# Kernel optimization log

Measured on AMD Instinct MI355X. Metric: run time of the kernel, lower is better.

Reference implementation:

```python
import jax, jax.numpy as jnp
import numpy as np

N, D = 16384, 256

def setup_inputs() -> dict:
    key = jax.random.key(0)
    k1, k2 = jax.random.split(key)
    image_emb = jax.random.normal(k1, (N, D), dtype=jnp.float32)
    text_emb = jax.random.normal(k2, (N, D), dtype=jnp.float32)
    return {"image_emb": image_emb, "text_emb": text_emb}

def reference(image_emb, text_emb):
    n = image_emb.shape[0]
    # [n, n] similarity logits
    logits = image_emb @ text_emb.T
    labels = jnp.arange(n)
    # cross-entropy with diagonal labels: -log_softmax(logits)[i, i]
    logp_t = jax.nn.log_softmax(logits, axis=-1)        # image -> text (rows)
    logp_i = jax.nn.log_softmax(logits.T, axis=-1)      # text -> image (cols)
    loss_t = -logp_t[labels, labels]
    loss_i = -logp_i[labels, labels]
    loss = ((loss_i + loss_t) * 0.5).mean()
    return loss
```

## Files before the change

kernel.cpp:

```cpp
#include <hip/hip_runtime.h>
#include <hip/hip_bf16.h>

#define NN 16384
#define DD 256

typedef unsigned short u16;
typedef unsigned int u32;
typedef unsigned char u8;
typedef long i64;
typedef __attribute__((ext_vector_type(4))) float f32x4;
typedef __attribute__((ext_vector_type(8))) int i32x8;

static __device__ __forceinline__ void gload16(const u8* g, u8* l) {
    __builtin_amdgcn_global_load_lds(
        (const __attribute__((address_space(1))) void*)g,
        (__attribute__((address_space(3))) void*)l,
        16, 0, 0);
}

__global__ void prep_kernel(const float* __restrict__ img, const float* __restrict__ txt,
                            u8* __restrict__ A8, u8* __restrict__ B8,
                            float* __restrict__ zbuf ,
                            float* __restrict__ out) {
    int gid = blockIdx.x * 256 + threadIdx.x;
    float4 va = ((const float4*)img)[gid];
    float4 vb = ((const float4*)txt)[gid];
    const float S = 1.44269504088896f;
    int pa = __builtin_amdgcn_cvt_pk_fp8_f32(va.x * S, va.y * S, 0, false);
    pa     = __builtin_amdgcn_cvt_pk_fp8_f32(va.z * S, va.w * S, pa, true);
    int pb = __builtin_amdgcn_cvt_pk_fp8_f32(vb.x, vb.y, 0, false);
    pb     = __builtin_amdgcn_cvt_pk_fp8_f32(vb.z, vb.w, pb, true);

    const int r  = gid >> 6;
    const int rl = r & 127;
    const int pn = r >> 7;
    const int ko = (gid & 63) << 2;
    const int kb = ko ^ ((rl & 15) << 3);
    *(u32*)(A8 + ((size_t)pn << 15) + (rl << 8) + kb) = (u32)pa;
    *(u32*)(B8 + ((size_t)pn << 15) + (rl << 8) + kb) = (u32)pb;
    if (gid < 32768) zbuf[gid] = 0.0f;
    if (gid == 0) out[0] = 0.0f;
}

__global__ __launch_bounds__(256, 2) void gemm_lse_kernel(
        const u8* __restrict__ A8, const u8* __restrict__ B8,
        float* __restrict__ s_row, float* __restrict__ s_col,
        float* __restrict__ diag) {
    __shared__ u8 sA[32768];
    __shared__ u8 sB[32768];

    const int t = threadIdx.x;
    const int lane = t & 63;
    const int w = t >> 6;
    const int wr = w >> 1, wc = w & 1;
    const int q = lane >> 4, m = lane & 15;
    const int bi = blockIdx.x & 127;
    const int jg = blockIdx.x >> 7;
    const int row0 = bi << 7;

    #pragma unroll
    for (int R = 0; R < 8; ++R)
        gload16(A8 + ((size_t)bi << 15) + (R << 12) + (w << 10) + ((size_t)lane << 4),
                &sA[(R << 12) + (w << 10)]);
    __syncthreads();

    i32x8 areg[2][4];
    #pragma unroll
    for (int k2 = 0; k2 < 2; ++k2)
        #pragma unroll
        for (int rb = 0; rb < 4; ++rb) {
            const int rr = (wr << 6) + (rb << 4) + m;
            union { i32x8 v; i64 d[4]; } ua;
            #pragma unroll
            for (int j = 0; j < 4; ++j)
                ua.d[j] = *(const i64*)(&sA[(rr << 8) + (k2 << 7)
                           + (((q << 5) | (j << 3)) ^ (m << 3))]);
            areg[k2][rb] = ua.v;
        }

    const f32x4 fzero = {0.f, 0.f, 0.f, 0.f};
    const f32x4 cinit = {-144.f, -144.f, -144.f, -144.f};
    f32x4 acc[4][4];
    f32x4 rp[4] = {fzero, fzero, fzero, fzero};

    #pragma unroll 1
    for (int jt = 0; jt < 16; ++jt) {
        const int ct = (jg << 4) | ((jt + bi) & 15);
        const int col0 = ct << 7;
        __syncthreads();
        #pragma unroll
        for (int R = 0; R < 8; ++R)
            gload16(B8 + ((size_t)ct << 15) + (R << 12) + (w << 10) + ((size_t)lane << 4),
                    &sB[(R << 12) + (w << 10)]);
        __syncthreads();

        #pragma unroll
        for (int k2 = 0; k2 < 2; ++k2) {
            i32x8 bf[4];
            #pragma unroll
            for (int cb = 0; cb < 4; ++cb) {
                const int cr = (wc << 6) + (cb << 4) + m;
                union { i32x8 v; i64 d[4]; } ub;
                #pragma unroll
                for (int j = 0; j < 4; ++j)
                    ub.d[j] = *(const i64*)(&sB[(cr << 8) + (k2 << 7)
                               + (((q << 5) | (j << 3)) ^ (m << 3))]);
                bf[cb] = ub.v;
            }
            if (k2 == 0) {
                #pragma unroll
                for (int rb = 0; rb < 4; ++rb)
                    #pragma unroll
                    for (int cb = 0; cb < 4; ++cb)
                        acc[rb][cb] = __builtin_amdgcn_mfma_scale_f32_16x16x128_f8f6f4(
                            areg[0][rb], bf[cb], cinit, 0, 0, 0, 127, 0, 127);
            } else {
                #pragma unroll
                for (int rb = 0; rb < 4; ++rb)
                    #pragma unroll
                    for (int cb = 0; cb < 4; ++cb)
                        acc[rb][cb] = __builtin_amdgcn_mfma_scale_f32_16x16x128_f8f6f4(
                            areg[1][rb], bf[cb], acc[rb][cb], 0, 0, 0, 127, 0, 127);
            }
        }

        if (bi == ct && wr == wc) {
            #pragma unroll
            for (int rb = 0; rb < 4; ++rb)
                #pragma unroll
                for (int r = 0; r < 4; ++r)
                    if (m == ((q << 2) | r))
                        diag[row0 + (wr << 6) + (rb << 4) + m] = acc[rb][rb][r];
        }
        #pragma unroll
        for (int rb = 0; rb < 4; ++rb)
            #pragma unroll
            for (int cb = 0; cb < 4; ++cb)
                #pragma unroll
                for (int r = 0; r < 4; ++r)
                    acc[rb][cb][r] = __builtin_amdgcn_exp2f(acc[rb][cb][r]);

        #pragma unroll
        for (int rb = 0; rb < 4; ++rb)
            rp[rb] += (acc[rb][0] + acc[rb][1]) + (acc[rb][2] + acc[rb][3]);

        float cpart = 0.0f;
        #pragma unroll
        for (int cb = 0; cb < 4; ++cb) {
            float v = 0.0f;
            #pragma unroll
            for (int rb = 0; rb < 4; ++rb)
                v += (acc[rb][cb][0] + acc[rb][cb][1]) + (acc[rb][cb][2] + acc[rb][cb][3]);
            v += __shfl_xor(v, 16, 64);
            v += __shfl_xor(v, 32, 64);
            if (q == cb) cpart = v;
        }
        atomicAdd(&s_col[col0 + (wc << 6) + (q << 4) + m], cpart);
    }

    float rout = 0.0f;
    #pragma unroll
    for (int rb = 0; rb < 4; ++rb)
        #pragma unroll
        for (int r = 0; r < 4; ++r) {
            float v = rp[rb][r];
            v += __shfl_xor(v, 1, 16);
            v += __shfl_xor(v, 2, 16);
            v += __shfl_xor(v, 4, 16);
            v += __shfl_xor(v, 8, 16);
            if (m == ((rb << 2) | r)) rout = v;
        }
    atomicAdd(&s_row[row0 + (wr << 6) + ((m >> 2) << 4) + (q << 2) + (m & 3)], rout);
}

__global__ void final_kernel(const float* __restrict__ s_row, const float* __restrict__ s_col,
                             const float* __restrict__ diag, float* __restrict__ out) {
    __shared__ double red[256];
    int t = threadIdx.x;
    int i = blockIdx.x * 256 + t;
    double p = 0.5 * (double)(log2f(s_row[i]) + log2f(s_col[i])) - (double)diag[i];
    red[t] = p;
    __syncthreads();
    for (int s = 128; s > 0; s >>= 1) {
        if (t < s) red[t] += red[t + s];
        __syncthreads();
    }
    if (t == 0) atomicAdd(out, (float)(red[0] * 0.6931471805599453 / (double)NN));
}

extern "C" void kernel_launch(void* const* d_in, const int* in_sizes, int n_in,
                              void* d_out, int out_size, void* d_ws, size_t ws_size,
                              hipStream_t stream) {
    const float* img = (const float*)d_in[0];
    const float* txt = (const float*)d_in[1];
    char* ws = (char*)d_ws;
    u8*    A8    = (u8*)ws;
    u8*    B8    = (u8*)(ws + 4194304);
    float* s_row = (float*)(ws + 8388608);
    float* s_col = (float*)(ws + 8388608 + 65536);
    float* diag  = (float*)(ws + 8388608 + 131072);
    float* out   = (float*)d_out;

    prep_kernel<<<4096, 256, 0, stream>>>(img, txt, A8, B8, s_row, out);
    gemm_lse_kernel<<<1024, 256, 0, stream>>>(A8, B8, s_row, s_col, diag);
    final_kernel<<<64, 256, 0, stream>>>(s_row, s_col, diag, out);
}
```

Before: 168.9 us.

## Load B fragments directly from global into registers with prefetch, dropping LDS staging

The prep kernel now writes B in a fragment-major layout so each lane can read its MFMA operand with two 16-byte global loads. The GEMM kernel drops the shared B buffer and both per-tile barriers, and instead loads B fragments straight into registers. It prefetches the next tile's first K-half while the current MFMAs run, and raises wave priority around the MFMA blocks. This removes LDS traffic and synchronization, but it raises register pressure and relies on L2 to serve B reuse, since each wave now re-reads B from global memory.

```diff
diff --git a/kernel.cpp b/kernel.cpp
--- a/kernel.cpp
+++ b/kernel.cpp
@@ -9,6 +9,7 @@
 typedef unsigned char u8;
 typedef long i64;
 typedef __attribute__((ext_vector_type(4))) float f32x4;
+typedef __attribute__((ext_vector_type(4))) int i32x4;
 typedef __attribute__((ext_vector_type(8))) int i32x8;
 
 static __device__ __forceinline__ void gload16(const u8* g, u8* l) {
@@ -35,9 +36,13 @@
     const int rl = r & 127;
     const int pn = r >> 7;
     const int ko = (gid & 63) << 2;
-    const int kb = ko ^ ((rl & 15) << 3);
-    *(u32*)(A8 + ((size_t)pn << 15) + (rl << 8) + kb) = (u32)pa;
-    *(u32*)(B8 + ((size_t)pn << 15) + (rl << 8) + kb) = (u32)pb;
+    const int kbA = ko ^ ((rl & 15) << 3);
+    *(u32*)(A8 + ((size_t)pn << 15) + (rl << 8) + kbA) = (u32)pa;
+    const int mm  = rl & 15, cb8 = rl >> 4;
+    const int k2  = ko >> 7, koo = ko & 127;
+    const int qq  = koo >> 5, jj = (koo >> 4) & 1, u = ko & 15;
+    *(u32*)(B8 + ((size_t)pn << 15) + (k2 << 14) + (cb8 << 11) + (jj << 10)
+               + (qq << 8) + (mm << 4) + u) = (u32)pb;
     if (gid < 32768) zbuf[gid] = 0.0f;
     if (gid == 0) out[0] = 0.0f;
 }
@@ -47,7 +52,6 @@
         float* __restrict__ s_row, float* __restrict__ s_col,
         float* __restrict__ diag) {
     __shared__ u8 sA[32768];
-    __shared__ u8 sB[32768];
 
     const int t = threadIdx.x;
     const int lane = t & 63;
@@ -83,46 +87,62 @@
     f32x4 acc[4][4];
     f32x4 rp[4] = {fzero, fzero, fzero, fzero};
 
+    const u8* Bw = B8 + (wc << 13) + ((size_t)lane << 4);
+
+    i32x8 bfA[4], bfB[4];
+
+    {
+        const int ct0 = (jg << 4) | (bi & 15);
+        const u8* p = Bw + ((size_t)ct0 << 15);
+        #pragma unroll
+        for (int cb = 0; cb < 4; ++cb) {
+            i32x4 lo = *(const i32x4*)(p + (cb << 11));
+            i32x4 hi = *(const i32x4*)(p + (cb << 11) + 1024);
+            bfA[cb] = __builtin_shufflevector(lo, hi, 0, 1, 2, 3, 4, 5, 6, 7);
+        }
+    }
+
     #pragma unroll 1
     for (int jt = 0; jt < 16; ++jt) {
         const int ct = (jg << 4) | ((jt + bi) & 15);
         const int col0 = ct << 7;
-        __syncthreads();
-        #pragma unroll
-        for (int R = 0; R < 8; ++R)
-            gload16(B8 + ((size_t)ct << 15) + (R << 12) + (w << 10) + ((size_t)lane << 4),
-                    &sB[(R << 12) + (w << 10)]);
-        __syncthreads();
-
-        #pragma unroll
-        for (int k2 = 0; k2 < 2; ++k2) {
-            i32x8 bf[4];
+        const u8* p = Bw + ((size_t)ct << 15);
+
+        #pragma unroll
+        for (int cb = 0; cb < 4; ++cb) {
+            i32x4 lo = *(const i32x4*)(p + 16384 + (cb << 11));
+            i32x4 hi = *(const i32x4*)(p + 16384 + (cb << 11) + 1024);
+            bfB[cb] = __builtin_shufflevector(lo, hi, 0, 1, 2, 3, 4, 5, 6, 7);
+        }
+
+        __builtin_amdgcn_s_setprio(1);
+        #pragma unroll
+        for (int rb = 0; rb < 4; ++rb)
+            #pragma unroll
+            for (int cb = 0; cb < 4; ++cb)
+                acc[rb][cb] = __builtin_amdgcn_mfma_scale_f32_16x16x128_f8f6f4(
+                    areg[0][rb], bfA[cb], cinit, 0, 0, 0, 127, 0, 127);
+        __builtin_amdgcn_s_setprio(0);
+
+        if (jt < 15) {
+            const int ctn = (jg << 4) | ((jt + 1 + bi) & 15);
+            const u8* pn2 = Bw + ((size_t)ctn << 15);
             #pragma unroll
             for (int cb = 0; cb < 4; ++cb) {
-                const int cr = (wc << 6) + (cb << 4) + m;
-                union { i32x8 v; i64 d[4]; } ub;
-                #pragma unroll
-                for (int j = 0; j < 4; ++j)
-                    ub.d[j] = *(const i64*)(&sB[(cr << 8) + (k2 << 7)
-                               + (((q << 5) | (j << 3)) ^ (m << 3))]);
-                bf[cb] = ub.v;
+                i32x4 lo = *(const i32x4*)(pn2 + (cb << 11));
+                i32x4 hi = *(const i32x4*)(pn2 + (cb << 11) + 1024);
+                bfA[cb] = __builtin_shufflevector(lo, hi, 0, 1, 2, 3, 4, 5, 6, 7);
             }
-            if (k2 == 0) {
-                #pragma unroll
-                for (int rb = 0; rb < 4; ++rb)
-                    #pragma unroll
-                    for (int cb = 0; cb < 4; ++cb)
-                        acc[rb][cb] = __builtin_amdgcn_mfma_scale_f32_16x16x128_f8f6f4(
-                            areg[0][rb], bf[cb], cinit, 0, 0, 0, 127, 0, 127);
-            } else {
-                #pragma unroll
-                for (int rb = 0; rb < 4; ++rb)
-                    #pragma unroll
-                    for (int cb = 0; cb < 4; ++cb)
-                        acc[rb][cb] = __builtin_amdgcn_mfma_scale_f32_16x16x128_f8f6f4(
-                            areg[1][rb], bf[cb], acc[rb][cb], 0, 0, 0, 127, 0, 127);
-            }
-        }
+        }
+
+        __builtin_amdgcn_s_setprio(1);
+        #pragma unroll
+        for (int rb = 0; rb < 4; ++rb)
+            #pragma unroll
+            for (int cb = 0; cb < 4; ++cb)
+                acc[rb][cb] = __builtin_amdgcn_mfma_scale_f32_16x16x128_f8f6f4(
+                    areg[1][rb], bfB[cb], acc[rb][cb], 0, 0, 0, 127, 0, 127);
+        __builtin_amdgcn_s_setprio(0);
 
         if (bi == ct && wr == wc) {
             #pragma unroll
```

New measurement: 151.0 us. 10.6% less time.
